# Kernel optimization log

Hardware: AMD Instinct MI355X
Metric: run time of the kernel (lower is better)

Reference implementation:

```python
import jax, jax.numpy as jnp
import numpy as np

NUM_HEADS = 4

def setup_inputs() -> dict:
    key = jax.random.key(0)
    ks = jax.random.split(key, 7)
    B, Lq, Lk, E, D, LAT = 16, 256, 4096, 64, 32, 32
    query = jax.random.normal(ks[0], (B, Lq, E), dtype=jnp.float32)
    key_in = jax.random.normal(ks[1], (B, Lk, E), dtype=jnp.float32)
    value = jax.random.normal(ks[2], (B, Lk, D), dtype=jnp.float32)
    mask = jax.random.randint(ks[3], (B, Lk, D), 0, 2, dtype=jnp.int32)
    Wq = jax.random.normal(ks[4], (E, E), dtype=jnp.float32) / np.sqrt(E).astype(np.float32)
    bq = jnp.zeros((E,), dtype=jnp.float32)
    Wk = jax.random.normal(ks[5], (E, E), dtype=jnp.float32) / np.sqrt(E).astype(np.float32)
    bk = jnp.zeros((E,), dtype=jnp.float32)
    Wo = jax.random.normal(ks[6], (NUM_HEADS * D, LAT), dtype=jnp.float32) / np.sqrt(NUM_HEADS * D).astype(np.float32)
    bo = jnp.zeros((LAT,), dtype=jnp.float32)
    return {"query": query, "key": key_in, "value": value, "mask": mask,
            "Wq": Wq, "bq": bq, "Wk": Wk, "bk": bk, "Wo": Wo, "bo": bo}

def reference(query, key, value, mask, Wq, bq, Wk, bk, Wo, bo):
    B, Lk, D = value.shape
    Lq = query.shape[1]
    h = NUM_HEADS
    ek = query.shape[-1] // h  # embed_time_k
    # linear maps (torch Linear: y = x @ W; here W stored as (in, out))
    q = (query @ Wq + bq).reshape(B, Lq, h, ek).transpose(0, 2, 1, 3)  # (B,h,Lq,ek)
    k = (key @ Wk + bk).reshape(B, Lk, h, ek).transpose(0, 2, 1, 3)    # (B,h,Lk,ek)
    scores = jnp.einsum('bhqe,bhke->bhqk', q, k) / jnp.sqrt(jnp.asarray(ek, q.dtype))
    # Original repeats scores over D, masks per-feature with -inf, softmaxes over Lk,
    # then does a weighted sum. Equivalent fused form (never builds (B,h,Lq,Lk,D)):
    e = jnp.exp(scores - jnp.max(scores, axis=-1, keepdims=True))  # (B,h,Lq,Lk)
    m = mask.astype(value.dtype)                                   # (B,Lk,D) 0/1
    num = jnp.einsum('bhqk,bkd->bhqd', e, m * value)
    den = jnp.einsum('bhqk,bkd->bhqd', e, m)
    x = num / den                                                  # (B,h,Lq,D)
    x = x.transpose(0, 2, 1, 3).reshape(B, Lq, h * D)
    return x @ Wo + bo  # (B, Lq, latent_dim)
```

## Files before the change

kernel.cpp:

```cpp
#include <hip/hip_runtime.h>
#include <hip/hip_bf16.h>

typedef __bf16 bf16;
typedef bf16 bf16x4 __attribute__((ext_vector_type(4)));
typedef bf16 bf16x8 __attribute__((ext_vector_type(8)));
typedef float f32x4 __attribute__((ext_vector_type(4)));

#define B_   16
#define LQ_  256
#define LK_  4096
#define E_   64
#define H_   4
#define EK_  16
#define D_   32
#define LAT_ 32

#define OFF_QP    0u
#define OFF_KP    524288u
#define OFF_MVFT  8912896u
#define OFF_WOT   17301504u
#define OFF_ND    17309696u
#define WS_NEED   21504000u

__device__ inline f32x4 mfma_bf16(bf16x8 a, bf16x8 b, f32x4 c) {
  return __builtin_amdgcn_mfma_f32_16x16x32_bf16(a, b, c, 0, 0, 0);
}
__device__ inline bf16x8 zero8() {
  bf16x8 z;
#pragma unroll
  for (int i = 0; i < 8; ++i) z[i] = (bf16)0.0f;
  return z;
}

__global__ __launch_bounds__(256) void prep_kernel(
    const float* __restrict__ query, const float* __restrict__ key,
    const float* __restrict__ value, const int* __restrict__ mask,
    const float* __restrict__ Wq, const float* __restrict__ bq,
    const float* __restrict__ Wk, const float* __restrict__ bk,
    const float* __restrict__ Wo,
    bf16* __restrict__ qp, bf16* __restrict__ kp,
    bf16* __restrict__ mvfT, bf16* __restrict__ WoT)
{
  __shared__ __align__(16) bf16 s_b[16896];
  const int bid = blockIdx.x;
  const int tid = threadIdx.x;

  if (bid < 544) {
    const bool isQ = bid < 32;
    const int row0 = isQ ? bid * 128 : (bid - 32) * 128;
    const float* in   = isQ ? query : key;
    const float* W    = isQ ? Wq : Wk;
    const float* bias = isQ ? bq : bk;
    bf16* outp        = isQ ? qp : kp;
    const float scal  = isQ ? 0.25f : 1.0f;

    bf16* sIn = s_b;
    bf16* sWT = s_b + 9216;

#pragma unroll
    for (int p = 0; p < 8; ++p) {
      int f4 = tid + p * 256;
      int row = f4 >> 4, e4 = (f4 & 15) * 4;
      float4 v = *(const float4*)(in + (size_t)(row0 + row) * 64 + e4);
      bf16x4 b4;
      b4[0] = (bf16)v.x; b4[1] = (bf16)v.y; b4[2] = (bf16)v.z; b4[3] = (bf16)v.w;
      *(bf16x4*)(sIn + row * 72 + e4) = b4;
    }
#pragma unroll
    for (int p = 0; p < 4; ++p) {
      int f4 = tid + p * 256;
      int k = f4 >> 4, c4 = (f4 & 15) * 4;
      float4 v = *(const float4*)(W + k * 64 + c4);
      sWT[(c4 + 0) * 72 + k] = (bf16)v.x;
      sWT[(c4 + 1) * 72 + k] = (bf16)v.y;
      sWT[(c4 + 2) * 72 + k] = (bf16)v.z;
      sWT[(c4 + 3) * 72 + k] = (bf16)v.w;
    }
    __syncthreads();

    const int w = tid >> 6, l = tid & 63, l15 = l & 15, g = l >> 4;
    f32x4 acc[2][4];
#pragma unroll
    for (int mt = 0; mt < 2; ++mt)
#pragma unroll
      for (int nt = 0; nt < 4; ++nt) acc[mt][nt] = f32x4{0.f, 0.f, 0.f, 0.f};

#pragma unroll
    for (int ks = 0; ks < 2; ++ks) {
      bf16x8 A0 = *(bf16x8*)(sIn + (32 * w + l15) * 72 + 32 * ks + 8 * g);
      bf16x8 A1 = *(bf16x8*)(sIn + (32 * w + 16 + l15) * 72 + 32 * ks + 8 * g);
#pragma unroll
      for (int nt = 0; nt < 4; ++nt) {
        bf16x8 Bf = *(bf16x8*)(sWT + (16 * nt + l15) * 72 + 32 * ks + 8 * g);
        acc[0][nt] = mfma_bf16(A0, Bf, acc[0][nt]);
        acc[1][nt] = mfma_bf16(A1, Bf, acc[1][nt]);
      }
    }
#pragma unroll
    for (int mt = 0; mt < 2; ++mt)
#pragma unroll
      for (int nt = 0; nt < 4; ++nt) {
        int col = 16 * nt + l15;
        float bv = bias[col];
#pragma unroll
        for (int r = 0; r < 4; ++r) {
          int row = row0 + 32 * w + 16 * mt + 4 * g + r;
          outp[(size_t)row * 64 + col] = (bf16)((acc[mt][nt][r] + bv) * scal);
        }
      }
  } else if (bid < 800) {
    const int rb = bid - 544;
    const int b = rb >> 4, kk0 = (rb & 15) * 256;
#pragma unroll
    for (int p = 0; p < 8; ++p) {
      int f4 = tid + p * 256;
      int kk = f4 >> 3, d4 = (f4 & 7) * 4;
      size_t gi = ((size_t)(b * LK_ + kk0 + kk)) * 32 + d4;
      float4 v = *(const float4*)(value + gi);
      int4   m = *(const int4*)(mask + gi);
      s_b[(d4 + 0) * 264 + kk] = (bf16)(m.x ? v.x : 0.0f);
      s_b[(d4 + 1) * 264 + kk] = (bf16)(m.y ? v.y : 0.0f);
      s_b[(d4 + 2) * 264 + kk] = (bf16)(m.z ? v.z : 0.0f);
      s_b[(d4 + 3) * 264 + kk] = (bf16)(m.w ? v.w : 0.0f);
      s_b[(32 + d4 + 0) * 264 + kk] = (bf16)(float)m.x;
      s_b[(32 + d4 + 1) * 264 + kk] = (bf16)(float)m.y;
      s_b[(32 + d4 + 2) * 264 + kk] = (bf16)(float)m.z;
      s_b[(32 + d4 + 3) * 264 + kk] = (bf16)(float)m.w;
    }
    __syncthreads();
    const int col = tid >> 2, seg = tid & 3;
#pragma unroll
    for (int w2 = 0; w2 < 8; ++w2) {
      uint4 d = *(uint4*)(s_b + col * 264 + seg * 64 + w2 * 8);
      *(uint4*)(mvfT + ((size_t)(b * 64 + col)) * LK_ + kk0 + seg * 64 + w2 * 8) = d;
    }
  } else {
#pragma unroll
    for (int p = 0; p < 16; ++p) {
      int f = tid + p * 256;
      int k = f >> 5, n = f & 31;
      WoT[n * 128 + k] = (bf16)Wo[f];
    }
  }
}

__global__ __launch_bounds__(256, 4) void attn_kernel(
    const bf16* __restrict__ qp, const bf16* __restrict__ kp,
    const bf16* __restrict__ mvfT, float* __restrict__ nd)
{
  __shared__ __align__(16) bf16 s_mv[2112];
  __shared__ __align__(16) bf16 s_se[5120];

  const int bid = blockIdx.x;
  const int kc = bid & 7, qt = (bid >> 3) & 7, b = bid >> 6;
  const int tid = threadIdx.x;
  const int w = tid >> 6, l = tid & 63, l15 = l & 15, g = l >> 4;
  const int q0 = qt * 32;
  const int kkb = kc * 512;

  bf16x8 qB[2];
  if (l < 32) {
#pragma unroll
    for (int nt = 0; nt < 2; ++nt) {
      int q = q0 + 16 * nt + l15;
      qB[nt] = *(const bf16x8*)(qp + (size_t)((b * LQ_ + q) * 64 + w * EK_ + g * 8));
    }
  } else { qB[0] = zero8(); qB[1] = zero8(); }

  f32x4 acc[2][4];
#pragma unroll
  for (int mt = 0; mt < 2; ++mt)
#pragma unroll
    for (int nt = 0; nt < 4; ++nt) acc[mt][nt] = f32x4{0.f, 0.f, 0.f, 0.f};

  const bf16* mv_src = mvfT + ((size_t)(b * 64 + (tid >> 2))) * LK_ + (tid & 3) * 8;
  bf16* mv_dst = s_mv + ((tid & 3) * 528 + (tid >> 2) * 8);
  bf16* se_w = s_se + w * 1280;

  for (int t = 0; t < 16; ++t) {
    const int kk0 = kkb + t * 32;
    uint4 mvld = *(const uint4*)(mv_src + kk0);
    bf16x8 kA0, kA1;
    if (l < 32) {
      kA0 = *(const bf16x8*)(kp + (size_t)((b * LK_ + kk0 + l15) * 64 + w * EK_ + g * 8));
      kA1 = *(const bf16x8*)(kp + (size_t)((b * LK_ + kk0 + 16 + l15) * 64 + w * EK_ + g * 8));
    } else { kA0 = zero8(); kA1 = zero8(); }

    __syncthreads();
    *(uint4*)mv_dst = mvld;

    f32x4 S[2][2];
    S[0][0] = mfma_bf16(kA0, qB[0], f32x4{0.f, 0.f, 0.f, 0.f});
    S[0][1] = mfma_bf16(kA0, qB[1], f32x4{0.f, 0.f, 0.f, 0.f});
    S[1][0] = mfma_bf16(kA1, qB[0], f32x4{0.f, 0.f, 0.f, 0.f});
    S[1][1] = mfma_bf16(kA1, qB[1], f32x4{0.f, 0.f, 0.f, 0.f});

#pragma unroll
    for (int mt = 0; mt < 2; ++mt)
#pragma unroll
      for (int nt = 0; nt < 2; ++nt) {
        f32x4 s = S[mt][nt];
        bf16x4 e4;
#pragma unroll
        for (int r = 0; r < 4; ++r) e4[r] = (bf16)__expf(s[r]);
        *(bf16x4*)(se_w + (16 * nt + l15) * 40 + 16 * mt + 4 * g) = e4;
      }

    asm volatile("" ::: "memory");

    bf16x8 eA0 = *(bf16x8*)(se_w + l15 * 40 + 8 * g);
    bf16x8 eA1 = *(bf16x8*)(se_w + (16 + l15) * 40 + 8 * g);

    __syncthreads();
#pragma unroll
    for (int nt = 0; nt < 4; ++nt) {
      bf16x8 mvB = *(bf16x8*)(s_mv + g * 528 + (l15 + 16 * nt) * 8);
      acc[0][nt] = mfma_bf16(eA0, mvB, acc[0][nt]);
      acc[1][nt] = mfma_bf16(eA1, mvB, acc[1][nt]);
    }
  }

#pragma unroll
  for (int mt = 0; mt < 2; ++mt)
#pragma unroll
    for (int nt = 0; nt < 4; ++nt)
#pragma unroll
      for (int r = 0; r < 4; ++r) {
        int q = q0 + 16 * mt + 4 * g + r;
        int col = 16 * nt + l15;
        atomicAdd(&nd[(size_t)((b * 4 + w) * LQ_ + q) * 64 + col], acc[mt][nt][r]);
      }
}

__global__ __launch_bounds__(256) void out_kernel(
    const float* __restrict__ nd, const bf16* __restrict__ WoT,
    const float* __restrict__ bo, float* __restrict__ out)
{
  __shared__ __align__(16) bf16 s_x[16 * 136];
  const int bid = blockIdx.x;
  const int b = bid >> 4, q0 = (bid & 15) * 16;
  const int tid = threadIdx.x;
  const int q = tid >> 4, jg = tid & 15;
#pragma unroll
  for (int jj = 0; jj < 8; ++jj) {
    int j = jg * 8 + jj;
    int h = j >> 5, d = j & 31;
    size_t base = (size_t)((b * 4 + h) * LQ_ + q0 + q) * 64;
    float num = nd[base + d], den = nd[base + 32 + d];
    s_x[q * 136 + j] = (bf16)(num / den);
  }
  __syncthreads();
  const int w = tid >> 6, l = tid & 63, l15 = l & 15, g = l >> 4;
  if (w < 2) {
    const int nt = w;
    f32x4 acc = f32x4{0.f, 0.f, 0.f, 0.f};
#pragma unroll
    for (int ks = 0; ks < 4; ++ks) {
      bf16x8 A  = *(bf16x8*)(s_x + l15 * 136 + 32 * ks + 8 * g);
      bf16x8 Bf = *(const bf16x8*)(WoT + (l15 + 16 * nt) * 128 + 32 * ks + 8 * g);
      acc = mfma_bf16(A, Bf, acc);
    }
    float bv = bo[l15 + 16 * nt];
#pragma unroll
    for (int r = 0; r < 4; ++r) {
      int row = q0 + 4 * g + r;
      out[(size_t)(b * LQ_ + row) * LAT_ + l15 + 16 * nt] = acc[r] + bv;
    }
  }
}

extern "C" void kernel_launch(void* const* d_in, const int* in_sizes, int n_in,
                              void* d_out, int out_size, void* d_ws, size_t ws_size,
                              hipStream_t stream) {
  const float* query = (const float*)d_in[0];
  const float* key   = (const float*)d_in[1];
  const float* value = (const float*)d_in[2];
  const int*   mask  = (const int*)d_in[3];
  const float* Wq    = (const float*)d_in[4];
  const float* bq    = (const float*)d_in[5];
  const float* Wk    = (const float*)d_in[6];
  const float* bk    = (const float*)d_in[7];
  const float* Wo    = (const float*)d_in[8];
  const float* bo    = (const float*)d_in[9];
  float* out = (float*)d_out;
  char* ws = (char*)d_ws;

  if (ws_size < (size_t)WS_NEED) return;

  bf16* qp   = (bf16*)(ws + OFF_QP);
  bf16* kp   = (bf16*)(ws + OFF_KP);
  bf16* mvfT = (bf16*)(ws + OFF_MVFT);
  bf16* WoT  = (bf16*)(ws + OFF_WOT);
  float* nd  = (float*)(ws + OFF_ND);

  hipMemsetAsync(nd, 0, 4194304u, stream);
  prep_kernel<<<801, 256, 0, stream>>>(query, key, value, mask, Wq, bq, Wk, bk,
                                       Wo, qp, kp, mvfT, WoT);
  attn_kernel<<<1024, 256, 0, stream>>>(qp, kp, mvfT, nd);
  out_kernel<<<256, 256, 0, stream>>>(nd, WoT, bo, out);
}
```

Measured before the change: 143.8 us.

## Pre-swizzle masked value tiles into MFMA fragment layout and drop LDS staging

The prep kernel now writes the masked-value/mask matrix directly in the per-lane MFMA B-fragment order for each 32-key tile. The attention kernel can then load its B operands straight from global memory into registers, which removes the shared-memory staging buffer and both block-wide barriers per iteration. It also folds log2(e) into the query scale so the kernel can use exp2f instead of __expf. The trade-off is that each wave redundantly loads the same value tile from global or L2 instead of sharing one LDS copy.

Result: faster. 139.7 us (-2.9%).

```diff
diff --git a/kernel.cpp b/kernel.cpp
--- a/kernel.cpp
+++ b/kernel.cpp
@@ -1,5 +1,6 @@
 #include <hip/hip_runtime.h>
 #include <hip/hip_bf16.h>
+#include <math.h>
 
 typedef __bf16 bf16;
 typedef bf16 bf16x4 __attribute__((ext_vector_type(4)));
@@ -17,10 +18,12 @@
 
 #define OFF_QP    0u
 #define OFF_KP    524288u
-#define OFF_MVFT  8912896u
+#define OFF_MVFB  8912896u
 #define OFF_WOT   17301504u
 #define OFF_ND    17309696u
 #define WS_NEED   21504000u
+
+#define LOG2E 1.44269504f
 
 __device__ inline f32x4 mfma_bf16(bf16x8 a, bf16x8 b, f32x4 c) {
   return __builtin_amdgcn_mfma_f32_16x16x32_bf16(a, b, c, 0, 0, 0);
@@ -39,7 +42,7 @@
     const float* __restrict__ Wk, const float* __restrict__ bk,
     const float* __restrict__ Wo,
     bf16* __restrict__ qp, bf16* __restrict__ kp,
-    bf16* __restrict__ mvfT, bf16* __restrict__ WoT)
+    bf16* __restrict__ mvfB, bf16* __restrict__ WoT)
 {
   __shared__ __align__(16) bf16 s_b[16896];
   const int bid = blockIdx.x;
@@ -52,7 +55,7 @@
     const float* W    = isQ ? Wq : Wk;
     const float* bias = isQ ? bq : bk;
     bf16* outp        = isQ ? qp : kp;
-    const float scal  = isQ ? 0.25f : 1.0f;
+    const float scal  = isQ ? (0.25f * LOG2E) : 1.0f;
 
     bf16* sIn = s_b;
     bf16* sWT = s_b + 9216;
@@ -129,10 +132,15 @@
     }
     __syncthreads();
     const int col = tid >> 2, seg = tid & 3;
+    const int nt = col >> 4, l15c = col & 15;
 #pragma unroll
     for (int w2 = 0; w2 < 8; ++w2) {
-      uint4 d = *(uint4*)(s_b + col * 264 + seg * 64 + w2 * 8);
-      *(uint4*)(mvfT + ((size_t)(b * 64 + col)) * LK_ + kk0 + seg * 64 + w2 * 8) = d;
+      int kkg = seg * 64 + w2 * 8;
+      int tile = (kk0 + kkg) >> 5;
+      int gq = (kkg >> 3) & 3;
+      int lane = 16 * gq + l15c;
+      uint4 d = *(uint4*)(s_b + col * 264 + kkg);
+      *(uint4*)(mvfB + (size_t)((((b * 128 + tile) * 4 + nt) * 64 + lane)) * 8) = d;
     }
   } else {
 #pragma unroll
@@ -146,9 +154,8 @@
 
 __global__ __launch_bounds__(256, 4) void attn_kernel(
     const bf16* __restrict__ qp, const bf16* __restrict__ kp,
-    const bf16* __restrict__ mvfT, float* __restrict__ nd)
+    const bf16* __restrict__ mvfB, float* __restrict__ nd)
 {
-  __shared__ __align__(16) bf16 s_mv[2112];
   __shared__ __align__(16) bf16 s_se[5120];
 
   const int bid = blockIdx.x;
@@ -156,7 +163,7 @@
   const int tid = threadIdx.x;
   const int w = tid >> 6, l = tid & 63, l15 = l & 15, g = l >> 4;
   const int q0 = qt * 32;
-  const int kkb = kc * 512;
+  const int tile0 = kc * 16;
 
   bf16x8 qB[2];
   if (l < 32) {
@@ -173,22 +180,25 @@
 #pragma unroll
     for (int nt = 0; nt < 4; ++nt) acc[mt][nt] = f32x4{0.f, 0.f, 0.f, 0.f};
 
-  const bf16* mv_src = mvfT + ((size_t)(b * 64 + (tid >> 2))) * LK_ + (tid & 3) * 8;
-  bf16* mv_dst = s_mv + ((tid & 3) * 528 + (tid >> 2) * 8);
   bf16* se_w = s_se + w * 1280;
-
+  const bf16* mvt0 = mvfB + (size_t)(b * 128 + tile0) * 2048;
+
+#pragma unroll 2
   for (int t = 0; t < 16; ++t) {
-    const int kk0 = kkb + t * 32;
-    uint4 mvld = *(const uint4*)(mv_src + kk0);
+    const int kk0 = (tile0 + t) * 32;
+    const bf16* mvt = mvt0 + (size_t)t * 2048;
+
+    bf16x8 mvB[4];
+#pragma unroll
+    for (int nt = 0; nt < 4; ++nt)
+      mvB[nt] = *(const bf16x8*)(mvt + (nt * 64 + l) * 8);
+
     bf16x8 kA0, kA1;
     if (l < 32) {
       kA0 = *(const bf16x8*)(kp + (size_t)((b * LK_ + kk0 + l15) * 64 + w * EK_ + g * 8));
       kA1 = *(const bf16x8*)(kp + (size_t)((b * LK_ + kk0 + 16 + l15) * 64 + w * EK_ + g * 8));
     } else { kA0 = zero8(); kA1 = zero8(); }
 
-    __syncthreads();
-    *(uint4*)mv_dst = mvld;
-
     f32x4 S[2][2];
     S[0][0] = mfma_bf16(kA0, qB[0], f32x4{0.f, 0.f, 0.f, 0.f});
     S[0][1] = mfma_bf16(kA0, qB[1], f32x4{0.f, 0.f, 0.f, 0.f});
@@ -202,7 +212,7 @@
         f32x4 s = S[mt][nt];
         bf16x4 e4;
 #pragma unroll
-        for (int r = 0; r < 4; ++r) e4[r] = (bf16)__expf(s[r]);
+        for (int r = 0; r < 4; ++r) e4[r] = (bf16)exp2f(s[r]);
         *(bf16x4*)(se_w + (16 * nt + l15) * 40 + 16 * mt + 4 * g) = e4;
       }
 
@@ -211,12 +221,10 @@
     bf16x8 eA0 = *(bf16x8*)(se_w + l15 * 40 + 8 * g);
     bf16x8 eA1 = *(bf16x8*)(se_w + (16 + l15) * 40 + 8 * g);
 
-    __syncthreads();
 #pragma unroll
     for (int nt = 0; nt < 4; ++nt) {
-      bf16x8 mvB = *(bf16x8*)(s_mv + g * 528 + (l15 + 16 * nt) * 8);
-      acc[0][nt] = mfma_bf16(eA0, mvB, acc[0][nt]);
-      acc[1][nt] = mfma_bf16(eA1, mvB, acc[1][nt]);
+      acc[0][nt] = mfma_bf16(eA0, mvB[nt], acc[0][nt]);
+      acc[1][nt] = mfma_bf16(eA1, mvB[nt], acc[1][nt]);
     }
   }
 
@@ -289,13 +297,13 @@
 
   bf16* qp   = (bf16*)(ws + OFF_QP);
   bf16* kp   = (bf16*)(ws + OFF_KP);
-  bf16* mvfT = (bf16*)(ws + OFF_MVFT);
+  bf16* mvfB = (bf16*)(ws + OFF_MVFB);
   bf16* WoT  = (bf16*)(ws + OFF_WOT);
   float* nd  = (float*)(ws + OFF_ND);
 
   hipMemsetAsync(nd, 0, 4194304u, stream);
   prep_kernel<<<801, 256, 0, stream>>>(query, key, value, mask, Wq, bq, Wk, bk,
-                                       Wo, qp, kp, mvfT, WoT);
-  attn_kernel<<<1024, 256, 0, stream>>>(qp, kp, mvfT, nd);
+                                       Wo, qp, kp, mvfB, WoT);
+  attn_kernel<<<1024, 256, 0, stream>>>(qp, kp, mvfB, nd);
   out_kernel<<<256, 256, 0, stream>>>(nd, WoT, bo, out);
 }
```
